# Kernel optimization log

Measured on AMD Instinct MI355X. Metric: run time of the kernel, lower is better.

Reference implementation:

```python
import jax, jax.numpy as jnp
import numpy as np


def setup_inputs() -> dict:
    key = jax.random.key(0)
    ks = jax.random.split(key, 8)
    b, s1, s2 = 16, 512, 40
    video_dim, text_dim, attn_dim = 1024, 300, 256
    return {
        "video": jax.random.normal(ks[0], (b, s1, video_dim), dtype=jnp.float32),
        "text": jax.random.normal(ks[1], (b, s2, text_dim), dtype=jnp.float32),
        "w1": jax.random.normal(ks[2], (video_dim, attn_dim), dtype=jnp.float32),
        "w2": jax.random.normal(ks[3], (text_dim, attn_dim), dtype=jnp.float32),
        "w3": jax.random.normal(ks[4], (attn_dim, 1), dtype=jnp.float32),
        "bias": jax.random.normal(ks[5], (attn_dim,), dtype=jnp.float32),
        "w4": jax.random.normal(ks[6], (4 * attn_dim, 500), dtype=jnp.float32),
        "b4": jax.random.normal(ks[7], (500,), dtype=jnp.float32),
    }


def reference(video, text, w1, w2, w3, bias, w4, b4):
    # video: (b, s1, d1), text: (b, s2, d2)
    e = jnp.einsum("bsd,da->bsa", video, w1)   # (b, s1, a) -- also 'hh' in original
    f = jnp.einsum("btd,da->bta", text, w2)    # (b, s2, a)
    # additive attention energies: tanh over (b, s1, s2, a) broadcast sum
    h = jnp.tanh(e[:, :, None, :] + f[:, None, :, :] + bias)  # (b, s1, s2, a)
    logits = jnp.squeeze(jnp.einsum("bsta,ao->bsto", h, w3), -1)  # (b, s1, s2)
    # original expands logits over attn_dim then softmaxes dim=2; identical to
    # softmax over s2 of the scalar scores, broadcast afterwards.
    attn = jax.nn.softmax(logits, axis=2)  # (b, s1, s2)
    text_attn = jnp.einsum("bst,bta->bsa", attn, f)  # (b, s1, a)
    cont = jnp.concatenate(
        [e, text_attn, e * text_attn, e - text_attn], axis=-1
    )  # (b, s1, 4a)
    return jnp.tanh(cont) @ w4 + b4  # (b, s1, 500)
```

## Files before the change

kernel.cpp:

```cpp
#include <hip/hip_runtime.h>
#include <hip/hip_bf16.h>
#include <cstdint>

typedef __attribute__((ext_vector_type(8))) short bf16x8;
typedef __attribute__((ext_vector_type(4))) short bf16x4;
typedef __attribute__((ext_vector_type(4))) float f32x4;

#define TANH_SCALE 2.8853900817779268f
#define TANH_UNSCALE 0.34657359027997264f

__device__ __forceinline__ short cvt_bf16(float f) {
  union { float f; uint32_t u; } x; x.f = f;
  uint32_t r = x.u + 0x7FFFu + ((x.u >> 16) & 1u);
  return (short)(r >> 16);
}
__device__ __forceinline__ float bf16_to_f(short s) {
  union { uint32_t u; float f; } x; x.u = ((uint32_t)(uint16_t)s) << 16;
  return x.f;
}

__device__ __forceinline__ float tanh_fast(float x) {
  float e = __builtin_amdgcn_exp2f(x * TANH_SCALE);
  return 1.0f - 2.0f * __builtin_amdgcn_rcpf(e + 1.0f);
}
__device__ __forceinline__ float sig_pre(float xs) {
  float e = __builtin_amdgcn_exp2f(xs);
  return __builtin_amdgcn_rcpf(e + 1.0f);
}

__device__ __forceinline__ void split8(float4 a, float4 b, bf16x8& h, bf16x8& l) {
  float fa[8] = {a.x, a.y, a.z, a.w, b.x, b.y, b.z, b.w};
  uint32_t uh[8], ul[8];
  #pragma unroll
  for (int j = 0; j < 8; j++) {
    union { float f; uint32_t u; } x; x.f = fa[j];
    uh[j] = x.u;
    union { uint32_t u; float f; } t; t.u = x.u & 0xffff0000u;
    union { float f; uint32_t u; } y; y.f = fa[j] - t.f;
    ul[j] = y.u;
  }
  union { uint32_t w[4]; bf16x8 v; } H, L;
  #pragma unroll
  for (int j = 0; j < 4; j++) {
    H.w[j] = __builtin_amdgcn_perm(uh[2 * j + 1], uh[2 * j], 0x07060302u);
    L.w[j] = __builtin_amdgcn_perm(ul[2 * j + 1], ul[2 * j], 0x07060302u);
  }
  h = H.v; l = L.v;
}

__global__ __launch_bounds__(256) void k_prep(const float* __restrict__ text,
                                              const float* __restrict__ w1,
                                              const float* __restrict__ w2,
                                              const float* __restrict__ w4,
                                              short* __restrict__ w1h,
                                              short* __restrict__ w1l,
                                              short* __restrict__ w4T,
                                              short* __restrict__ th,
                                              short* __restrict__ tl,
                                              short* __restrict__ w2h,
                                              short* __restrict__ w2l) {
  __shared__ float tile[32][33];
  int bid = blockIdx.x;
  if (bid < 256) {
    int idx = bid;
    int r0 = (idx & 31) * 32, c0 = (idx >> 5) * 32;
    int j = threadIdx.x & 31, i0 = threadIdx.x >> 5;
    #pragma unroll
    for (int i = i0; i < 32; i += 8) tile[i][j] = w1[(size_t)(r0 + i) * 256 + c0 + j];
    __syncthreads();
    #pragma unroll
    for (int i = i0; i < 32; i += 8) {
      float v = tile[j][i];
      short h = cvt_bf16(v);
      w1h[(size_t)(c0 + i) * 1024 + r0 + j] = h;
      w1l[(size_t)(c0 + i) * 1024 + r0 + j] = cvt_bf16(v - bf16_to_f(h));
    }
  } else if (bid < 768) {
    int idx = bid - 256;
    int r0 = (idx & 31) * 32, c0 = (idx >> 5) * 32;
    int j = threadIdx.x & 31, i0 = threadIdx.x >> 5;
    #pragma unroll
    for (int i = i0; i < 32; i += 8) {
      int c = c0 + j;
      tile[i][j] = (c < 500) ? w4[(size_t)(r0 + i) * 500 + c] : 0.f;
    }
    __syncthreads();
    #pragma unroll
    for (int i = i0; i < 32; i += 8)
      w4T[(size_t)(c0 + i) * 1024 + r0 + j] = cvt_bf16(tile[j][i]);
  } else if (bid < 928) {
    int idx = bid - 768;
    int row = idx * 4 + (threadIdx.x >> 6);
    int cl = threadIdx.x & 63;
    const float* trow = text + (size_t)row * 300;
    short* hrow = th + (size_t)row * 320;
    short* lrow = tl + (size_t)row * 320;
    #pragma unroll
    for (int c0 = 0; c0 < 320; c0 += 64) {
      int c = c0 + cl;
      float v = (c < 300) ? trow[c] : 0.f;
      short h = cvt_bf16(v);
      hrow[c] = h;
      lrow[c] = cvt_bf16(v - bf16_to_f(h));
    }
  } else {
    int idx = bid - 928;
    int rt = idx % 10, ct = idx / 10;
    int r0 = rt * 32, c0 = ct * 32;
    int j = threadIdx.x & 31, i0 = threadIdx.x >> 5;
    #pragma unroll
    for (int i = i0; i < 32; i += 8) {
      int r = r0 + i;
      tile[i][j] = (r < 300) ? w2[(size_t)r * 256 + c0 + j] : 0.f;
    }
    __syncthreads();
    #pragma unroll
    for (int i = i0; i < 32; i += 8) {
      float v = tile[j][i];
      short h = cvt_bf16(v);
      w2h[(size_t)(c0 + i) * 320 + r0 + j] = h;
      w2l[(size_t)(c0 + i) * 320 + r0 + j] = cvt_bf16(v - bf16_to_f(h));
    }
  }
}

__device__ __forceinline__ void load_lds16(void* lds, const void* g) {
  __builtin_amdgcn_global_load_lds(
      (const __attribute__((address_space(1))) void*)g,
      (__attribute__((address_space(3))) void*)lds, 16, 0, 0);
}

__global__ __launch_bounds__(256) void k_gemm_big(const float* __restrict__ video,
                                                  const short* __restrict__ w1h,
                                                  const short* __restrict__ w1l,
                                                  const short* __restrict__ th,
                                                  const short* __restrict__ tl,
                                                  const short* __restrict__ w2h,
                                                  const short* __restrict__ w2l,
                                                  float* __restrict__ eparts,
                                                  float* __restrict__ fbuf) {
  __shared__ __align__(16) char smem[49152];
  int bid = blockIdx.x;
  int tid = threadIdx.x, lane = tid & 63, wave = tid >> 6;
  int mrow = lane & 15, quad = lane >> 4;

  if (bid < 512) {
    short (*Ash)[64] = (short (*)[64])(smem);
    short (*Asl)[64] = (short (*)[64])(smem + 16384);
    short (*Bsh)[64] = (short (*)[64])(smem + 32768);
    short (*Bsl)[64] = (short (*)[64])(smem + 40960);
    int m0 = (bid & 63) * 128, n0 = ((bid >> 6) & 3) * 64;
    int z = bid >> 8;
    int kz0 = z * 512;
    int wm = wave * 32;
    int lrow = lane >> 3, lseg = (lane & 7) * 8;

    f32x4 acc[2][4];
    #pragma unroll
    for (int i = 0; i < 2; i++)
      #pragma unroll
      for (int j = 0; j < 4; j++) acc[i][j] = (f32x4){0.f, 0.f, 0.f, 0.f};

    float4 va[8];
    #pragma unroll
    for (int it = 0; it < 4; it++) {
      int idx = it * 256 + tid;
      const float* src = video + (size_t)(m0 + (idx >> 3)) * 1024 + kz0 + (idx & 7) * 8;
      va[it * 2]     = *(const float4*)src;
      va[it * 2 + 1] = *(const float4*)(src + 4);
    }

    for (int k0 = kz0; k0 < kz0 + 512; k0 += 64) {
      bf16x8 hi[4], lo[4];
      #pragma unroll
      for (int it = 0; it < 4; it++) split8(va[it * 2], va[it * 2 + 1], hi[it], lo[it]);
      __syncthreads();
      #pragma unroll
      for (int it = 0; it < 4; it++) {
        int idx = it * 256 + tid;
        *(bf16x8*)&Ash[idx >> 3][(idx & 7) * 8] = hi[it];
        *(bf16x8*)&Asl[idx >> 3][(idx & 7) * 8] = lo[it];
      }
      #pragma unroll
      for (int i = 0; i < 2; i++) {
        int c = wave * 2 + i;
        size_t go = (size_t)(n0 + c * 8 + lrow) * 1024 + k0 + lseg;
        load_lds16(&Bsh[c * 8][0], w1h + go);
        load_lds16(&Bsl[c * 8][0], w1l + go);
      }
      if (k0 + 64 < kz0 + 512) {
        #pragma unroll
        for (int it = 0; it < 4; it++) {
          int idx = it * 256 + tid;
          const float* src = video + (size_t)(m0 + (idx >> 3)) * 1024 + (k0 + 64) + (idx & 7) * 8;
          va[it * 2]     = *(const float4*)src;
          va[it * 2 + 1] = *(const float4*)(src + 4);
        }
      }
      __syncthreads();
      #pragma unroll
      for (int ks = 0; ks < 2; ks++) {
        int kk = ks * 32 + quad * 8;
        bf16x8 ah[2], al[2], bh[4], bl[4];
        #pragma unroll
        for (int i = 0; i < 2; i++) {
          ah[i] = *(const bf16x8*)&Ash[wm + i * 16 + mrow][kk];
          al[i] = *(const bf16x8*)&Asl[wm + i * 16 + mrow][kk];
        }
        #pragma unroll
        for (int j = 0; j < 4; j++) {
          bh[j] = *(const bf16x8*)&Bsh[j * 16 + mrow][kk];
          bl[j] = *(const bf16x8*)&Bsl[j * 16 + mrow][kk];
        }
        #pragma unroll
        for (int i = 0; i < 2; i++)
          #pragma unroll
          for (int j = 0; j < 4; j++) {
            acc[i][j] = __builtin_amdgcn_mfma_f32_16x16x32_bf16(ah[i], bh[j], acc[i][j], 0, 0, 0);
            acc[i][j] = __builtin_amdgcn_mfma_f32_16x16x32_bf16(ah[i], bl[j], acc[i][j], 0, 0, 0);
            acc[i][j] = __builtin_amdgcn_mfma_f32_16x16x32_bf16(al[i], bh[j], acc[i][j], 0, 0, 0);
          }
      }
    }
    float* C = eparts + (size_t)z * 8192 * 256;
    int rbase = quad * 4;
    #pragma unroll
    for (int i = 0; i < 2; i++)
      #pragma unroll
      for (int j = 0; j < 4; j++) {
        int col = n0 + j * 16 + mrow;
        #pragma unroll
        for (int r = 0; r < 4; r++) {
          int row = m0 + wm + i * 16 + rbase + r;
          C[(size_t)row * 256 + col] = acc[i][j][r];
        }
      }
  } else {
    short (*Ash)[72] = (short (*)[72])(smem);
    short (*Asl)[72] = (short (*)[72])(smem + 9216);
    short (*Bsh)[72] = (short (*)[72])(smem + 18432);
    short (*Bsl)[72] = (short (*)[72])(smem + 27648);
    int idx = bid - 512;
    int m0 = (idx % 10) * 64, n0 = (idx / 10) * 64;
    int wm = (wave & 1) * 32, wn = (wave >> 1) * 32;
    int srow = tid >> 3, sseg = (tid & 7) * 8;
    f32x4 acc[2][2];
    #pragma unroll
    for (int i = 0; i < 2; i++)
      #pragma unroll
      for (int j = 0; j < 2; j++) acc[i][j] = (f32x4){0.f, 0.f, 0.f, 0.f};

    for (int k0 = 0; k0 < 320; k0 += 64) {
      size_t aoff0 = (size_t)(m0 + srow) * 320 + k0 + sseg;
      size_t aoff1 = aoff0 + (size_t)32 * 320;
      size_t boff0 = (size_t)(n0 + srow) * 320 + k0 + sseg;
      size_t boff1 = boff0 + (size_t)32 * 320;
      bf16x8 a0h = *(const bf16x8*)(th + aoff0);
      bf16x8 a1h = *(const bf16x8*)(th + aoff1);
      bf16x8 a0l = *(const bf16x8*)(tl + aoff0);
      bf16x8 a1l = *(const bf16x8*)(tl + aoff1);
      bf16x8 b0h = *(const bf16x8*)(w2h + boff0);
      bf16x8 b1h = *(const bf16x8*)(w2h + boff1);
      bf16x8 b0l = *(const bf16x8*)(w2l + boff0);
      bf16x8 b1l = *(const bf16x8*)(w2l + boff1);
      __syncthreads();
      *(bf16x8*)&Ash[srow][sseg] = a0h;  *(bf16x8*)&Ash[srow + 32][sseg] = a1h;
      *(bf16x8*)&Asl[srow][sseg] = a0l;  *(bf16x8*)&Asl[srow + 32][sseg] = a1l;
      *(bf16x8*)&Bsh[srow][sseg] = b0h;  *(bf16x8*)&Bsh[srow + 32][sseg] = b1h;
      *(bf16x8*)&Bsl[srow][sseg] = b0l;  *(bf16x8*)&Bsl[srow + 32][sseg] = b1l;
      __syncthreads();
      #pragma unroll
      for (int ks = 0; ks < 2; ks++) {
        int kk = ks * 32 + quad * 8;
        bf16x8 ah[2], al[2], bh[2], bl[2];
        ah[0] = *(const bf16x8*)&Ash[wm + mrow][kk];
        ah[1] = *(const bf16x8*)&Ash[wm + 16 + mrow][kk];
        al[0] = *(const bf16x8*)&Asl[wm + mrow][kk];
        al[1] = *(const bf16x8*)&Asl[wm + 16 + mrow][kk];
        bh[0] = *(const bf16x8*)&Bsh[wn + mrow][kk];
        bh[1] = *(const bf16x8*)&Bsh[wn + 16 + mrow][kk];
        bl[0] = *(const bf16x8*)&Bsl[wn + mrow][kk];
        bl[1] = *(const bf16x8*)&Bsl[wn + 16 + mrow][kk];
        #pragma unroll
        for (int i = 0; i < 2; i++)
          #pragma unroll
          for (int j = 0; j < 2; j++) {
            acc[i][j] = __builtin_amdgcn_mfma_f32_16x16x32_bf16(ah[i], bh[j], acc[i][j], 0, 0, 0);
            acc[i][j] = __builtin_amdgcn_mfma_f32_16x16x32_bf16(ah[i], bl[j], acc[i][j], 0, 0, 0);
            acc[i][j] = __builtin_amdgcn_mfma_f32_16x16x32_bf16(al[i], bh[j], acc[i][j], 0, 0, 0);
          }
      }
    }
    int rbase = quad * 4;
    #pragma unroll
    for (int i = 0; i < 2; i++)
      #pragma unroll
      for (int j = 0; j < 2; j++) {
        int col = n0 + wn + j * 16 + mrow;
        #pragma unroll
        for (int r = 0; r < 4; r++) {
          int row = m0 + wm + i * 16 + rbase + r;
          fbuf[(size_t)row * 256 + col] = acc[i][j][r];
        }
      }
  }
}

__global__ __launch_bounds__(256) void k_gemm_f(const short* __restrict__ A,
                                                const short* __restrict__ BT,
                                                const float* __restrict__ bias,
                                                float* __restrict__ C,
                                                int K, int ldc, int nstore) {
  __shared__ __align__(16) short As[128][64];
  __shared__ __align__(16) short Bs[64][64];
  int m0 = blockIdx.x * 128, n0 = blockIdx.y * 64;
  int tid = threadIdx.x, lane = tid & 63, wave = tid >> 6;
  int wm = wave * 32;
  int mrow = lane & 15, quad = lane >> 4;
  int lrow = lane >> 3, lseg = (lane & 7) * 8;

  f32x4 acc[2][4];
  #pragma unroll
  for (int i = 0; i < 2; i++)
    #pragma unroll
    for (int j = 0; j < 4; j++) acc[i][j] = (f32x4){0.f, 0.f, 0.f, 0.f};

  for (int k0 = 0; k0 < K; k0 += 64) {
    __syncthreads();
    #pragma unroll
    for (int i = 0; i < 4; i++) {
      int c = wave * 4 + i;
      load_lds16(&As[c * 8][0], A + (size_t)(m0 + c * 8 + lrow) * K + k0 + lseg);
    }
    #pragma unroll
    for (int i = 0; i < 2; i++) {
      int c = wave * 2 + i;
      load_lds16(&Bs[c * 8][0], BT + (size_t)(n0 + c * 8 + lrow) * K + k0 + lseg);
    }
    __syncthreads();
    #pragma unroll
    for (int ks = 0; ks < 2; ks++) {
      int kk = ks * 32 + quad * 8;
      bf16x8 af[2], bf[4];
      #pragma unroll
      for (int i = 0; i < 2; i++) af[i] = *(const bf16x8*)&As[wm + i * 16 + mrow][kk];
      #pragma unroll
      for (int j = 0; j < 4; j++) bf[j] = *(const bf16x8*)&Bs[j * 16 + mrow][kk];
      #pragma unroll
      for (int i = 0; i < 2; i++)
        #pragma unroll
        for (int j = 0; j < 4; j++)
          acc[i][j] = __builtin_amdgcn_mfma_f32_16x16x32_bf16(af[i], bf[j], acc[i][j], 0, 0, 0);
    }
  }
  int rbase = quad * 4;
  #pragma unroll
  for (int i = 0; i < 2; i++)
    #pragma unroll
    for (int j = 0; j < 4; j++) {
      int col = n0 + j * 16 + mrow;
      if (col < nstore) {
        float bv = bias[col];
        #pragma unroll
        for (int r = 0; r < 4; r++) {
          int row = m0 + wm + i * 16 + rbase + r;
          C[(size_t)row * ldc + col] = acc[i][j][r] + bv;
        }
      }
    }
}

__global__ __launch_bounds__(512) void k_middle(const float* __restrict__ e0p,
                                                const float* __restrict__ e1p,
                                                const float* __restrict__ fb,
                                                const float* __restrict__ w3,
                                                const float* __restrict__ bias,
                                                short* __restrict__ cont) {
  __shared__ __align__(16) float fbs[40 * 256];
  __shared__ float lg[16][40];
  __shared__ float attn[16][40];
  int tid = threadIdx.x, wave = tid >> 6, lane = tid & 63;
  int la = lane & 31, half = lane >> 5;
  int row0 = blockIdx.x * 16;
  int b = row0 >> 9;
  int lgrow = wave + (half ? 8 : 0);
  int myrow = row0 + lgrow;

  const float4* fsrc = (const float4*)(fb + (size_t)b * 40 * 256);
  const float4* bias4 = (const float4*)bias;
  for (int i = tid; i < 40 * 64; i += 512) {
    float4 v = fsrc[i];
    float4 bb = bias4[i & 63];
    v.x = (v.x + bb.x) * TANH_SCALE; v.y = (v.y + bb.y) * TANH_SCALE;
    v.z = (v.z + bb.z) * TANH_SCALE; v.w = (v.w + bb.w) * TANH_SCALE;
    ((float4*)fbs)[i] = v;
  }
  __syncthreads();

  int a0 = la * 8;
  size_t eoff = (size_t)myrow * 256 + a0;
  float4 p00 = *(const float4*)(e0p + eoff);
  float4 p01 = *(const float4*)(e0p + eoff + 4);
  float4 p10 = *(const float4*)(e1p + eoff);
  float4 p11 = *(const float4*)(e1p + eoff + 4);
  float4 e0, e1;
  e0.x = p00.x + p10.x; e0.y = p00.y + p10.y; e0.z = p00.z + p10.z; e0.w = p00.w + p10.w;
  e1.x = p01.x + p11.x; e1.y = p01.y + p11.y; e1.z = p01.z + p11.z; e1.w = p01.w + p11.w;
  float4 w30 = *(const float4*)(w3 + a0);
  float4 w31 = *(const float4*)(w3 + a0 + 4);
  w30.x *= -2.f; w30.y *= -2.f; w30.z *= -2.f; w30.w *= -2.f;
  w31.x *= -2.f; w31.y *= -2.f; w31.z *= -2.f; w31.w *= -2.f;
  float4 bv0 = *(const float4*)(bias + a0);
  float4 bv1 = *(const float4*)(bias + a0 + 4);
  float4 es0, es1;
  es0.x = e0.x * TANH_SCALE; es0.y = e0.y * TANH_SCALE;
  es0.z = e0.z * TANH_SCALE; es0.w = e0.w * TANH_SCALE;
  es1.x = e1.x * TANH_SCALE; es1.y = e1.y * TANH_SCALE;
  es1.z = e1.z * TANH_SCALE; es1.w = e1.w * TANH_SCALE;

  for (int tc = 0; tc < 40; tc += 4) {
    float p[4];
    #pragma unroll
    for (int u = 0; u < 4; u++) {
      const float* fr = &fbs[(tc + u) * 256 + a0];
      float4 f0 = *(const float4*)fr;
      float4 f1 = *(const float4*)(fr + 4);
      p[u] = sig_pre(es0.x + f0.x) * w30.x + sig_pre(es0.y + f0.y) * w30.y
           + sig_pre(es0.z + f0.z) * w30.z + sig_pre(es0.w + f0.w) * w30.w
           + sig_pre(es1.x + f1.x) * w31.x + sig_pre(es1.y + f1.y) * w31.y
           + sig_pre(es1.z + f1.z) * w31.z + sig_pre(es1.w + f1.w) * w31.w;
    }
    #pragma unroll
    for (int s = 16; s >= 1; s >>= 1) {
      #pragma unroll
      for (int u = 0; u < 4; u++) p[u] += __shfl_xor(p[u], s, 64);
    }
    if (la == 0) {
      #pragma unroll
      for (int u = 0; u < 4; u++) lg[lgrow][tc + u] = p[u];
    }
  }

  auto softmax_row = [&](int r) {
    float x = (lane < 40) ? lg[r][lane] : -3.0e38f;
    float m = x;
    #pragma unroll
    for (int s = 32; s >= 1; s >>= 1) m = fmaxf(m, __shfl_xor(m, s, 64));
    float ex = (lane < 40) ? __builtin_amdgcn_exp2f((x - m) * 1.4426950408889634f) : 0.f;
    float ssum = ex;
    #pragma unroll
    for (int s = 32; s >= 1; s >>= 1) ssum += __shfl_xor(ssum, s, 64);
    if (lane < 40) attn[r][lane] = ex * __builtin_amdgcn_rcpf(ssum);
  };
  softmax_row(wave);
  softmax_row(wave + 8);

  float ac[8] = {0.f,0.f,0.f,0.f,0.f,0.f,0.f,0.f};
  for (int t = 0; t < 40; t++) {
    float w = attn[lgrow][t];
    const float* fr = &fbs[t * 256 + a0];
    float4 f0 = *(const float4*)fr;
    float4 f1 = *(const float4*)(fr + 4);
    ac[0] += w * f0.x; ac[1] += w * f0.y; ac[2] += w * f0.z; ac[3] += w * f0.w;
    ac[4] += w * f1.x; ac[5] += w * f1.y; ac[6] += w * f1.z; ac[7] += w * f1.w;
  }
  float tx[8];
  tx[0] = ac[0] * TANH_UNSCALE - bv0.x; tx[1] = ac[1] * TANH_UNSCALE - bv0.y;
  tx[2] = ac[2] * TANH_UNSCALE - bv0.z; tx[3] = ac[3] * TANH_UNSCALE - bv0.w;
  tx[4] = ac[4] * TANH_UNSCALE - bv1.x; tx[5] = ac[5] * TANH_UNSCALE - bv1.y;
  tx[6] = ac[6] * TANH_UNSCALE - bv1.z; tx[7] = ac[7] * TANH_UNSCALE - bv1.w;
  float ev[8] = {e0.x, e0.y, e0.z, e0.w, e1.x, e1.y, e1.z, e1.w};

  short* crow = cont + (size_t)myrow * 1024 + a0;
  auto st8 = [&](int off, const float* v) {
    bf16x8 pk;
    #pragma unroll
    for (int i = 0; i < 8; i++) pk[i] = cvt_bf16(v[i]);
    *(bf16x8*)(crow + off) = pk;
  };
  float s0[8], s1[8], s2[8], s3[8];
  #pragma unroll
  for (int i = 0; i < 8; i++) {
    s0[i] = tanh_fast(ev[i]);
    s1[i] = tanh_fast(tx[i]);
    s2[i] = tanh_fast(ev[i] * tx[i]);
    s3[i] = tanh_fast(ev[i] - tx[i]);
  }
  st8(0, s0); st8(256, s1); st8(512, s2); st8(768, s3);
}

extern "C" void kernel_launch(void* const* d_in, const int* in_sizes, int n_in,
                              void* d_out, int out_size, void* d_ws, size_t ws_size,
                              hipStream_t stream) {
  const float* video = (const float*)d_in[0];
  const float* text  = (const float*)d_in[1];
  const float* w1    = (const float*)d_in[2];
  const float* w2    = (const float*)d_in[3];
  const float* w3    = (const float*)d_in[4];
  const float* bias  = (const float*)d_in[5];
  const float* w4    = (const float*)d_in[6];
  const float* b4    = (const float*)d_in[7];
  float* out = (float*)d_out;
  char* ws = (char*)d_ws;

  short* contbuf  = (short*)(ws);
  short* w1T_hi   = (short*)(ws + 16777216);
  short* w1T_lo   = (short*)(ws + 17301504);
  short* w4T      = (short*)(ws + 17825792);
  float* fbuf     = (float*)(ws + 18874368);
  float* eparts   = (float*)(ws + 19529728);
  float* epart1   = (float*)(ws + 19529728 + 8388608);
  short* text_hi  = (short*)(ws + 36306944);
  short* text_lo  = (short*)(ws + 36716544);
  short* w2T_hi   = (short*)(ws + 37126144);
  short* w2T_lo   = (short*)(ws + 37330944);

  k_prep<<<1008, 256, 0, stream>>>(text, w1, w2, w4,
                                   w1T_hi, w1T_lo, w4T,
                                   text_hi, text_lo, w2T_hi, w2T_lo);
  k_gemm_big<<<552, 256, 0, stream>>>(video, w1T_hi, w1T_lo,
                                      text_hi, text_lo, w2T_hi, w2T_lo,
                                      eparts, fbuf);
  k_middle<<<512, 512, 0, stream>>>(eparts, epart1, fbuf, w3, bias, contbuf);
  k_gemm_f<<<dim3(64, 8), 256, 0, stream>>>(contbuf, w4T, b4, out, 1024, 500, 500);
}
```

Baseline: 164.6 us.

## Double-buffer LDS tiles with async global-to-LDS prefetch in GEMM kernels

Both the big e/f GEMM kernel and the generic bf16 GEMM now keep two LDS buffers for the B tiles (and, in k_gemm_f, for A as well). The next K-tile is issued with global_load_lds before computing on the current one, and explicit vmcnt waits plus raw s_barrier replace the old __syncthreads pairs. The aim is to hide global-memory latency behind MFMA work. The cost is more LDS per block (64KB, and double the tile space in k_gemm_f), which may lower occupancy, and the hand-counted vmcnt values must match the number of outstanding loads.

```diff
diff --git a/kernel.cpp b/kernel.cpp
--- a/kernel.cpp
+++ b/kernel.cpp
@@ -139,7 +139,7 @@
                                                   const short* __restrict__ w2l,
                                                   float* __restrict__ eparts,
                                                   float* __restrict__ fbuf) {
-  __shared__ __align__(16) char smem[49152];
+  __shared__ __align__(16) char smem[65536];
   int bid = blockIdx.x;
   int tid = threadIdx.x, lane = tid & 63, wave = tid >> 6;
   int mrow = lane & 15, quad = lane >> 4;
@@ -147,8 +147,6 @@
   if (bid < 512) {
     short (*Ash)[64] = (short (*)[64])(smem);
     short (*Asl)[64] = (short (*)[64])(smem + 16384);
-    short (*Bsh)[64] = (short (*)[64])(smem + 32768);
-    short (*Bsl)[64] = (short (*)[64])(smem + 40960);
     int m0 = (bid & 63) * 128, n0 = ((bid >> 6) & 3) * 64;
     int z = bid >> 8;
     int kz0 = z * 512;
@@ -161,43 +159,55 @@
       #pragma unroll
       for (int j = 0; j < 4; j++) acc[i][j] = (f32x4){0.f, 0.f, 0.f, 0.f};
 
+    auto stageB = [&](int k0, int buf) {
+      short* Bh = (short*)(smem + 32768 + buf * 8192);
+      short* Bl = (short*)(smem + 49152 + buf * 8192);
+      #pragma unroll
+      for (int i = 0; i < 2; i++) {
+        int c = wave * 2 + i;
+        size_t go = (size_t)(n0 + c * 8 + lrow) * 1024 + k0 + lseg;
+        load_lds16(Bh + (size_t)(c * 8) * 64, w1h + go);
+        load_lds16(Bl + (size_t)(c * 8) * 64, w1l + go);
+      }
+    };
+    auto loadA = [&](int k0, float4* va) {
+      #pragma unroll
+      for (int it = 0; it < 4; it++) {
+        int idx = it * 256 + tid;
+        const float* src = video + (size_t)(m0 + (idx >> 3)) * 1024 + k0 + (idx & 7) * 8;
+        va[it * 2]     = *(const float4*)src;
+        va[it * 2 + 1] = *(const float4*)(src + 4);
+      }
+    };
+
     float4 va[8];
-    #pragma unroll
-    for (int it = 0; it < 4; it++) {
-      int idx = it * 256 + tid;
-      const float* src = video + (size_t)(m0 + (idx >> 3)) * 1024 + kz0 + (idx & 7) * 8;
-      va[it * 2]     = *(const float4*)src;
-      va[it * 2 + 1] = *(const float4*)(src + 4);
-    }
-
-    for (int k0 = kz0; k0 < kz0 + 512; k0 += 64) {
+    stageB(kz0, 0);
+    loadA(kz0, va);
+
+    for (int t = 0; t < 8; t++) {
+      int k0 = kz0 + t * 64;
+      int cur = t & 1;
       bf16x8 hi[4], lo[4];
       #pragma unroll
       for (int it = 0; it < 4; it++) split8(va[it * 2], va[it * 2 + 1], hi[it], lo[it]);
-      __syncthreads();
+      __builtin_amdgcn_s_barrier();
       #pragma unroll
       for (int it = 0; it < 4; it++) {
         int idx = it * 256 + tid;
         *(bf16x8*)&Ash[idx >> 3][(idx & 7) * 8] = hi[it];
         *(bf16x8*)&Asl[idx >> 3][(idx & 7) * 8] = lo[it];
       }
-      #pragma unroll
-      for (int i = 0; i < 2; i++) {
-        int c = wave * 2 + i;
-        size_t go = (size_t)(n0 + c * 8 + lrow) * 1024 + k0 + lseg;
-        load_lds16(&Bsh[c * 8][0], w1h + go);
-        load_lds16(&Bsl[c * 8][0], w1l + go);
-      }
-      if (k0 + 64 < kz0 + 512) {
-        #pragma unroll
-        for (int it = 0; it < 4; it++) {
-          int idx = it * 256 + tid;
-          const float* src = video + (size_t)(m0 + (idx >> 3)) * 1024 + (k0 + 64) + (idx & 7) * 8;
-          va[it * 2]     = *(const float4*)src;
-          va[it * 2 + 1] = *(const float4*)(src + 4);
-        }
-      }
-      __syncthreads();
+      if (t + 1 < 8) {
+        stageB(k0 + 64, cur ^ 1);
+        loadA(k0 + 64, va);
+        asm volatile("s_waitcnt vmcnt(12)" ::: "memory");
+      } else {
+        asm volatile("s_waitcnt vmcnt(0)" ::: "memory");
+      }
+      asm volatile("s_waitcnt lgkmcnt(0)" ::: "memory");
+      __builtin_amdgcn_s_barrier();
+      const short* Bh = (const short*)(smem + 32768 + cur * 8192);
+      const short* Bl = (const short*)(smem + 49152 + cur * 8192);
       #pragma unroll
       for (int ks = 0; ks < 2; ks++) {
         int kk = ks * 32 + quad * 8;
@@ -209,8 +219,8 @@
         }
         #pragma unroll
         for (int j = 0; j < 4; j++) {
-          bh[j] = *(const bf16x8*)&Bsh[j * 16 + mrow][kk];
-          bl[j] = *(const bf16x8*)&Bsl[j * 16 + mrow][kk];
+          bh[j] = *(const bf16x8*)&Bh[(size_t)(j * 16 + mrow) * 64 + kk];
+          bl[j] = *(const bf16x8*)&Bl[(size_t)(j * 16 + mrow) * 64 + kk];
         }
         #pragma unroll
         for (int i = 0; i < 2; i++)
@@ -311,8 +321,8 @@
                                                 const float* __restrict__ bias,
                                                 float* __restrict__ C,
                                                 int K, int ldc, int nstore) {
-  __shared__ __align__(16) short As[128][64];
-  __shared__ __align__(16) short Bs[64][64];
+  __shared__ __align__(16) short As[2][128][64];
+  __shared__ __align__(16) short Bs[2][64][64];
   int m0 = blockIdx.x * 128, n0 = blockIdx.y * 64;
   int tid = threadIdx.x, lane = tid & 63, wave = tid >> 6;
   int wm = wave * 32;
@@ -325,33 +335,45 @@
     #pragma unroll
     for (int j = 0; j < 4; j++) acc[i][j] = (f32x4){0.f, 0.f, 0.f, 0.f};
 
-  for (int k0 = 0; k0 < K; k0 += 64) {
-    __syncthreads();
+  auto stage = [&](int k0, int buf) {
     #pragma unroll
     for (int i = 0; i < 4; i++) {
       int c = wave * 4 + i;
-      load_lds16(&As[c * 8][0], A + (size_t)(m0 + c * 8 + lrow) * K + k0 + lseg);
+      load_lds16(&As[buf][c * 8][0], A + (size_t)(m0 + c * 8 + lrow) * K + k0 + lseg);
     }
     #pragma unroll
     for (int i = 0; i < 2; i++) {
       int c = wave * 2 + i;
-      load_lds16(&Bs[c * 8][0], BT + (size_t)(n0 + c * 8 + lrow) * K + k0 + lseg);
-    }
-    __syncthreads();
+      load_lds16(&Bs[buf][c * 8][0], BT + (size_t)(n0 + c * 8 + lrow) * K + k0 + lseg);
+    }
+  };
+
+  int NT = K >> 6;
+  stage(0, 0);
+  for (int t = 0; t < NT; t++) {
+    int cur = t & 1;
+    if (t + 1 < NT) {
+      stage((t + 1) << 6, cur ^ 1);
+      asm volatile("s_waitcnt vmcnt(6)" ::: "memory");
+    } else {
+      asm volatile("s_waitcnt vmcnt(0)" ::: "memory");
+    }
+    __builtin_amdgcn_s_barrier();
     #pragma unroll
     for (int ks = 0; ks < 2; ks++) {
       int kk = ks * 32 + quad * 8;
       bf16x8 af[2], bf[4];
       #pragma unroll
-      for (int i = 0; i < 2; i++) af[i] = *(const bf16x8*)&As[wm + i * 16 + mrow][kk];
-      #pragma unroll
-      for (int j = 0; j < 4; j++) bf[j] = *(const bf16x8*)&Bs[j * 16 + mrow][kk];
+      for (int i = 0; i < 2; i++) af[i] = *(const bf16x8*)&As[cur][wm + i * 16 + mrow][kk];
+      #pragma unroll
+      for (int j = 0; j < 4; j++) bf[j] = *(const bf16x8*)&Bs[cur][j * 16 + mrow][kk];
       #pragma unroll
       for (int i = 0; i < 2; i++)
         #pragma unroll
         for (int j = 0; j < 4; j++)
           acc[i][j] = __builtin_amdgcn_mfma_f32_16x16x32_bf16(af[i], bf[j], acc[i][j], 0, 0, 0);
     }
+    __builtin_amdgcn_s_barrier();
   }
   int rbase = quad * 4;
   #pragma unroll
```

New measurement: 163.7 us. About the same (-0.5%).
